# Kernel tuning notes

Hardware: AMD Instinct MI355X
Metric: run time of the kernel (lower is better)

## Reference

```python
import jax, jax.numpy as jnp
import numpy as np

N, M = 4096, 8192
IN_DIM, OUT_DIM = 4096, 1024
NUM_SAMPLE = 10


def setup_inputs() -> dict:
    key = jax.random.key(0)
    k1, k2, k3, k4, k5 = jax.random.split(key, 5)
    node_features = jax.random.normal(k1, (N, IN_DIM), dtype=jnp.float32)
    neighbor_features = jax.random.normal(k2, (M, IN_DIM), dtype=jnp.float32)
    # Xavier-ish scale for params
    weight = jax.random.normal(k3, (OUT_DIM, IN_DIM), dtype=jnp.float32) * (1.0 / np.sqrt(IN_DIM))
    attention_vector = jax.random.normal(k4, (2 * OUT_DIM, 1), dtype=jnp.float32) * 0.05
    neighbor_idx = jax.random.randint(k5, (N, NUM_SAMPLE), 0, M, dtype=jnp.int32)
    return {
        "node_features": node_features,
        "neighbor_features": neighbor_features,
        "weight": weight,
        "attention_vector": attention_vector,
        "neighbor_idx": neighbor_idx,
    }


def reference(node_features, neighbor_features, weight, attention_vector, neighbor_idx):
    # Linear transform: [N, out], [M, out]
    node_t = node_features @ weight.T
    neigh_t = neighbor_features @ weight.T

    # combined @ attention_vector decomposes:
    # cat([h_i, h_j]) @ a == h_i @ a1 + h_j @ a2  (same math, no [N,M,2*out] tensor)
    a1 = attention_vector[:OUT_DIM, 0]   # [out]
    a2 = attention_vector[OUT_DIM:, 0]   # [out]
    scores = jax.nn.leaky_relu((node_t @ a1)[:, None] + (neigh_t @ a2)[None, :],
                               negative_slope=0.2)  # [N, M]

    # Build dense 0/1 mask from sampled neighbor indices (ragged -> dense)
    rows = jnp.arange(N, dtype=jnp.int32)[:, None]                  # [N,1]
    mask = jnp.zeros((N, M), dtype=jnp.float32).at[rows, neighbor_idx].set(1.0)

    scores = jnp.where(mask == 0, -jnp.inf, scores)
    attn = jax.nn.softmax(scores, axis=1)           # masked softmax over neighbor pool
    return attn @ neigh_t                           # [N, out]
```

## Files before the change

kernel.cpp:

```cpp
#include <hip/hip_runtime.h>

#define IN_DIM  4096
#define OUT_DIM 1024
#define NN      4096
#define MM      8192
#define NSAMP   10

typedef __bf16 bf16x8 __attribute__((ext_vector_type(8)));
typedef float  fx4    __attribute__((ext_vector_type(4)));

__device__ __forceinline__ ushort f2bf(float f) {
    union { float f; unsigned u; } v; v.f = f;
    unsigned u = v.u;
    return (ushort)((u + 0x7FFFu + ((u >> 16) & 1u)) >> 16);
}
__device__ __forceinline__ float bf2f(ushort u) {
    union { unsigned u; float f; } v; v.u = ((unsigned)u) << 16;
    return v.f;
}

#define GLDS(g, l) __builtin_amdgcn_global_load_lds(                           \
    (const __attribute__((address_space(1))) unsigned*)(g),                    \
    (__attribute__((address_space(3))) unsigned*)(l), 16, 0, 0)

__global__ __launch_bounds__(256) void k_attvec(const float* __restrict__ W,
                                                const float* __restrict__ att,
                                                float* __restrict__ v1,
                                                float* __restrict__ v2,
                                                ushort* __restrict__ Wbf) {
    int k  = blockIdx.x * 256 + threadIdx.x;
    int o0 = blockIdx.y * 64;
    float s1 = 0.f, s2 = 0.f;
    for (int o = o0; o < o0 + 64; ++o) {
        float w = W[(size_t)o * IN_DIM + k];
        Wbf[(size_t)o * IN_DIM + k] = f2bf(w);
        s1 += att[o] * w;
        s2 += att[OUT_DIM + o] * w;
    }
    atomicAdd(&v1[k], s1);
    atomicAdd(&v2[k], s2);
}

__global__ __launch_bounds__(256) void k_rows(const float* __restrict__ node_f,
                                              const float* __restrict__ neigh_f,
                                              const float* __restrict__ v1,
                                              const float* __restrict__ v2,
                                              float* __restrict__ nalpha,
                                              float* __restrict__ nbeta,
                                              ushort* __restrict__ Abf) {
    int row = blockIdx.x;
    float s = 0.f;
    if (row < NN) {
        const float4* xr = reinterpret_cast<const float4*>(node_f + (size_t)row * IN_DIM);
        const float4* vr = reinterpret_cast<const float4*>(v1);
        for (int i = threadIdx.x; i < IN_DIM / 4; i += 256) {
            float4 a = xr[i], b = vr[i];
            s += a.x * b.x + a.y * b.y + a.z * b.z + a.w * b.w;
        }
    } else {
        int j = row - NN;
        const float4* xr = reinterpret_cast<const float4*>(neigh_f + (size_t)j * IN_DIM);
        const float4* vr = reinterpret_cast<const float4*>(v2);
        ushort4* yr = reinterpret_cast<ushort4*>(Abf + (size_t)j * IN_DIM);
        for (int i = threadIdx.x; i < IN_DIM / 4; i += 256) {
            float4 a = xr[i], b = vr[i];
            s += a.x * b.x + a.y * b.y + a.z * b.z + a.w * b.w;
            ushort4 o;
            o.x = f2bf(a.x); o.y = f2bf(a.y); o.z = f2bf(a.z); o.w = f2bf(a.w);
            yr[i] = o;
        }
    }
    for (int off = 32; off > 0; off >>= 1) s += __shfl_down(s, off, 64);
    __shared__ float ws[4];
    if ((threadIdx.x & 63) == 0) ws[threadIdx.x >> 6] = s;
    __syncthreads();
    if (threadIdx.x == 0) {
        float t = ws[0] + ws[1] + ws[2] + ws[3];
        if (row < NN) nalpha[row] = t; else nbeta[row - NN] = t;
    }
}

#define TM 128
#define TN 128
#define BK 32
#define KSPLIT (IN_DIM / 2)

__global__ __launch_bounds__(256, 4) void k_gemm(const ushort* __restrict__ A,
                                                 const ushort* __restrict__ B,
                                                 ushort* __restrict__ P) {
    __shared__ __align__(16) ushort As[TM * BK];
    __shared__ __align__(16) ushort Bs[TN * BK];
    const int tid  = threadIdx.x;
    const int lane = tid & 63;
    const int wave = tid >> 6;
    const int wm   = (wave >> 1) * 64;
    const int wn   = (wave & 1) * 64;
    const int bm   = blockIdx.x * TM;
    const int bn   = blockIdx.y * TN;
    const int kb   = blockIdx.z * KSPLIT;
    const int quad = lane >> 4;
    const int lrow = lane & 15;

    const int srow  = wave * 32 + (lane >> 2);
    const int skoff = (lane & 3) * 8;
    const ushort* gA = A + (size_t)(bm + srow) * IN_DIM + kb + skoff;
    const ushort* gB = B + (size_t)(bn + srow) * IN_DIM + kb + skoff;
    ushort* lA = As + wave * 1024;
    ushort* lB = Bs + wave * 1024;

    fx4 acc[4][4] = {};

    for (int k0 = 0; k0 < KSPLIT; k0 += BK) {
        GLDS(gA + k0,                lA);
        GLDS(gA + k0 + 16 * IN_DIM,  lA + 512);
        GLDS(gB + k0,                lB);
        GLDS(gB + k0 + 16 * IN_DIM,  lB + 512);
        __syncthreads();

        bf16x8 af[4], bfr[4];
#pragma unroll
        for (int mi = 0; mi < 4; ++mi)
            af[mi] = *reinterpret_cast<const bf16x8*>(As + (wm + mi * 16 + lrow) * BK + quad * 8);
#pragma unroll
        for (int ni = 0; ni < 4; ++ni)
            bfr[ni] = *reinterpret_cast<const bf16x8*>(Bs + (wn + ni * 16 + lrow) * BK + quad * 8);
#pragma unroll
        for (int mi = 0; mi < 4; ++mi)
#pragma unroll
            for (int ni = 0; ni < 4; ++ni)
                acc[mi][ni] = __builtin_amdgcn_mfma_f32_16x16x32_bf16(af[mi], bfr[ni], acc[mi][ni], 0, 0, 0);
        __syncthreads();
    }

    ushort* Pz = P + (size_t)blockIdx.z * MM * OUT_DIM;
#pragma unroll
    for (int mi = 0; mi < 4; ++mi)
#pragma unroll
        for (int ni = 0; ni < 4; ++ni) {
            int r = bm + wm + mi * 16 + quad * 4;
            int c = bn + wn + ni * 16 + lrow;
#pragma unroll
            for (int v = 0; v < 4; ++v)
                Pz[(size_t)(r + v) * OUT_DIM + c] = f2bf(acc[mi][ni][v]);
        }
}

__global__ __launch_bounds__(256) void k_aggregate(const ushort* __restrict__ P,
                                                   const float* __restrict__ nalpha,
                                                   const float* __restrict__ nbeta,
                                                   const int* __restrict__ nidx,
                                                   float* __restrict__ outp) {
    int row = blockIdx.x;
    __shared__ int   s_idx[NSAMP];
    __shared__ float s_w[NSAMP];
    if (threadIdx.x < 16) {
        int t = threadIdx.x;
        int j = (t < NSAMP) ? nidx[row * NSAMP + t] : -1;
        float score = -INFINITY;
        if (t < NSAMP) {
            float x = nalpha[row] + nbeta[j];
            score = x > 0.f ? x : 0.2f * x;
        }
        bool dup = false;
#pragma unroll
        for (int sIdx = 0; sIdx < NSAMP; ++sIdx) {
            int js = __shfl(j, sIdx, 16);
            if (sIdx < t && js == j) dup = true;
        }
        float mx = score;
#pragma unroll
        for (int off = 8; off > 0; off >>= 1) {
            float o = __shfl_xor(mx, off, 16);
            mx = o > mx ? o : mx;
        }
        float e = (t < NSAMP && !dup) ? expf(score - mx) : 0.f;
        float sum = e;
#pragma unroll
        for (int off = 8; off > 0; off >>= 1) sum += __shfl_xor(sum, off, 16);
        if (t < NSAMP) {
            s_idx[t] = j;
            s_w[t]   = e / sum;
        }
    }
    __syncthreads();
    int col = threadIdx.x * 4;
    float ax = 0.f, ay = 0.f, az = 0.f, aw = 0.f;
#pragma unroll
    for (int t = 0; t < NSAMP; ++t) {
        float w = s_w[t];
        size_t off = (size_t)s_idx[t] * OUT_DIM + col;
        ushort4 u0 = *reinterpret_cast<const ushort4*>(P + off);
        ushort4 u1 = *reinterpret_cast<const ushort4*>(P + (size_t)MM * OUT_DIM + off);
        ax += w * (bf2f(u0.x) + bf2f(u1.x));
        ay += w * (bf2f(u0.y) + bf2f(u1.y));
        az += w * (bf2f(u0.z) + bf2f(u1.z));
        aw += w * (bf2f(u0.w) + bf2f(u1.w));
    }
    float4 o; o.x = ax; o.y = ay; o.z = az; o.w = aw;
    *reinterpret_cast<float4*>(outp + (size_t)row * OUT_DIM + col) = o;
}

extern "C" void kernel_launch(void* const* d_in, const int* in_sizes, int n_in,
                              void* d_out, int out_size, void* d_ws, size_t ws_size,
                              hipStream_t stream) {
    const float* node_f  = (const float*)d_in[0];
    const float* neigh_f = (const float*)d_in[1];
    const float* W       = (const float*)d_in[2];
    const float* att     = (const float*)d_in[3];
    const int*   nidx    = (const int*)d_in[4];
    float* outp = (float*)d_out;

    char* ws = (char*)d_ws;
    ushort* Abf = (ushort*)ws;
    ushort* Wbf = (ushort*)(ws + 67108864);
    ushort* P   = (ushort*)(ws + 75497472);
    float*  v1     = (float*)(ws + 109051904);
    float*  v2     = v1 + IN_DIM;
    float*  nalpha = v2 + IN_DIM;
    float*  nbeta  = nalpha + NN;

    hipMemsetAsync(v1, 0, 2 * IN_DIM * sizeof(float), stream);

    k_attvec   <<<dim3(16, 16), 256, 0, stream>>>(W, att, v1, v2, Wbf);
    k_rows     <<<NN + MM,      256, 0, stream>>>(node_f, neigh_f, v1, v2, nalpha, nbeta, Abf);
    k_gemm     <<<dim3(MM / TM, OUT_DIM / TN, 2), 256, 0, stream>>>(Abf, Wbf, P);
    k_aggregate<<<NN,           256, 0, stream>>>(P, nalpha, nbeta, nidx, outp);
}
```

Measured before the change: 379.9 us.

## Retune prep kernels and restructure GEMM with BK64, LDS swizzle and block remap

The GEMM k-tile grows from 32 to 64, and LDS columns are XOR-swizzled to avoid bank conflicts on fragment reads. The 3D grid becomes a 1D grid with a remapping that interleaves workgroups, likely to spread them across XCDs for L2 locality. The row-reduction kernel now processes one row per wave, which removes the shared-memory reduction and the block barrier. The attvec kernel uses more blocks with fewer rows each to raise parallelism, at the cost of more atomics. Larger LDS tiles may reduce occupancy.

```diff
diff --git a/kernel.cpp b/kernel.cpp
--- a/kernel.cpp
+++ b/kernel.cpp
@@ -29,9 +29,10 @@
                                                 float* __restrict__ v2,
                                                 ushort* __restrict__ Wbf) {
     int k  = blockIdx.x * 256 + threadIdx.x;
-    int o0 = blockIdx.y * 64;
+    int o0 = blockIdx.y * 16;
     float s1 = 0.f, s2 = 0.f;
-    for (int o = o0; o < o0 + 64; ++o) {
+#pragma unroll
+    for (int o = o0; o < o0 + 16; ++o) {
         float w = W[(size_t)o * IN_DIM + k];
         Wbf[(size_t)o * IN_DIM + k] = f2bf(w);
         s1 += att[o] * w;
@@ -48,12 +49,14 @@
                                               float* __restrict__ nalpha,
                                               float* __restrict__ nbeta,
                                               ushort* __restrict__ Abf) {
-    int row = blockIdx.x;
+    int row  = blockIdx.x * 4 + (threadIdx.x >> 6);
+    int lane = threadIdx.x & 63;
     float s = 0.f;
     if (row < NN) {
         const float4* xr = reinterpret_cast<const float4*>(node_f + (size_t)row * IN_DIM);
         const float4* vr = reinterpret_cast<const float4*>(v1);
-        for (int i = threadIdx.x; i < IN_DIM / 4; i += 256) {
+#pragma unroll
+        for (int i = lane; i < IN_DIM / 4; i += 64) {
             float4 a = xr[i], b = vr[i];
             s += a.x * b.x + a.y * b.y + a.z * b.z + a.w * b.w;
         }
@@ -62,7 +65,8 @@
         const float4* xr = reinterpret_cast<const float4*>(neigh_f + (size_t)j * IN_DIM);
         const float4* vr = reinterpret_cast<const float4*>(v2);
         ushort4* yr = reinterpret_cast<ushort4*>(Abf + (size_t)j * IN_DIM);
-        for (int i = threadIdx.x; i < IN_DIM / 4; i += 256) {
+#pragma unroll
+        for (int i = lane; i < IN_DIM / 4; i += 64) {
             float4 a = xr[i], b = vr[i];
             s += a.x * b.x + a.y * b.y + a.z * b.z + a.w * b.w;
             ushort4 o;
@@ -70,19 +74,16 @@
             yr[i] = o;
         }
     }
+#pragma unroll
     for (int off = 32; off > 0; off >>= 1) s += __shfl_down(s, off, 64);
-    __shared__ float ws[4];
-    if ((threadIdx.x & 63) == 0) ws[threadIdx.x >> 6] = s;
-    __syncthreads();
-    if (threadIdx.x == 0) {
-        float t = ws[0] + ws[1] + ws[2] + ws[3];
-        if (row < NN) nalpha[row] = t; else nbeta[row - NN] = t;
+    if (lane == 0) {
+        if (row < NN) nalpha[row] = s; else nbeta[row - NN] = s;
     }
 }
 
 #define TM 128
 #define TN 128
-#define BK 32
+#define BK 64
 #define KSPLIT (IN_DIM / 2)
 
 __global__ __launch_bounds__(256, 4) void k_gemm(const ushort* __restrict__ A,
@@ -95,49 +96,63 @@
     const int wave = tid >> 6;
     const int wm   = (wave >> 1) * 64;
     const int wn   = (wave & 1) * 64;
-    const int bm   = blockIdx.x * TM;
-    const int bn   = blockIdx.y * TN;
-    const int kb   = blockIdx.z * KSPLIT;
-    const int quad = lane >> 4;
     const int lrow = lane & 15;
-
-    const int srow  = wave * 32 + (lane >> 2);
-    const int skoff = (lane & 3) * 8;
-    const ushort* gA = A + (size_t)(bm + srow) * IN_DIM + kb + skoff;
-    const ushort* gB = B + (size_t)(bn + srow) * IN_DIM + kb + skoff;
-    ushort* lA = As + wave * 1024;
-    ushort* lB = Bs + wave * 1024;
+    const int q    = lane >> 4;
+
+    const int bid = blockIdx.x;
+    const int wg  = (bid & 7) * 128 + (bid >> 3);
+    const int bx  = wg & 63;
+    const int by  = (wg >> 6) & 7;
+    const int bz  = wg >> 9;
+    const int bm  = bx * TM;
+    const int bn  = by * TN;
+    const int kb  = bz * KSPLIT;
+
+    const int sr  = wave * 32 + (lane >> 3);
+    const int sco = (((lane & 7) ^ (lane >> 3)) << 3);
+    const ushort* gA = A + (size_t)(bm + sr) * IN_DIM + kb + sco;
+    const ushort* gB = B + (size_t)(bn + sr) * IN_DIM + kb + sco;
+    ushort* lA = As + wave * 2048;
+    ushort* lB = Bs + wave * 2048;
+
+    const int c0u = ((q ^ (lrow & 7)) << 3);
 
     fx4 acc[4][4] = {};
 
     for (int k0 = 0; k0 < KSPLIT; k0 += BK) {
-        GLDS(gA + k0,                lA);
-        GLDS(gA + k0 + 16 * IN_DIM,  lA + 512);
-        GLDS(gB + k0,                lB);
-        GLDS(gB + k0 + 16 * IN_DIM,  lB + 512);
+#pragma unroll
+        for (int i = 0; i < 4; ++i)
+            GLDS(gA + k0 + (size_t)i * 8 * IN_DIM, lA + i * 512);
+#pragma unroll
+        for (int i = 0; i < 4; ++i)
+            GLDS(gB + k0 + (size_t)i * 8 * IN_DIM, lB + i * 512);
         __syncthreads();
 
-        bf16x8 af[4], bfr[4];
-#pragma unroll
-        for (int mi = 0; mi < 4; ++mi)
-            af[mi] = *reinterpret_cast<const bf16x8*>(As + (wm + mi * 16 + lrow) * BK + quad * 8);
-#pragma unroll
-        for (int ni = 0; ni < 4; ++ni)
-            bfr[ni] = *reinterpret_cast<const bf16x8*>(Bs + (wn + ni * 16 + lrow) * BK + quad * 8);
-#pragma unroll
-        for (int mi = 0; mi < 4; ++mi)
+#pragma unroll
+        for (int s = 0; s < 2; ++s) {
+            const int co = c0u ^ (s << 5);
+            bf16x8 af[4], bfr[4];
+#pragma unroll
+            for (int mi = 0; mi < 4; ++mi)
+                af[mi] = *reinterpret_cast<const bf16x8*>(As + (wm + mi * 16 + lrow) * BK + co);
 #pragma unroll
             for (int ni = 0; ni < 4; ++ni)
-                acc[mi][ni] = __builtin_amdgcn_mfma_f32_16x16x32_bf16(af[mi], bfr[ni], acc[mi][ni], 0, 0, 0);
+                bfr[ni] = *reinterpret_cast<const bf16x8*>(Bs + (wn + ni * 16 + lrow) * BK + co);
+#pragma unroll
+            for (int mi = 0; mi < 4; ++mi)
+#pragma unroll
+                for (int ni = 0; ni < 4; ++ni)
+                    acc[mi][ni] = __builtin_amdgcn_mfma_f32_16x16x32_bf16(af[mi], bfr[ni], acc[mi][ni], 0, 0, 0);
+        }
         __syncthreads();
     }
 
-    ushort* Pz = P + (size_t)blockIdx.z * MM * OUT_DIM;
+    ushort* Pz = P + (size_t)bz * MM * OUT_DIM;
 #pragma unroll
     for (int mi = 0; mi < 4; ++mi)
 #pragma unroll
         for (int ni = 0; ni < 4; ++ni) {
-            int r = bm + wm + mi * 16 + quad * 4;
+            int r = bm + wm + mi * 16 + q * 4;
             int c = bn + wn + ni * 16 + lrow;
 #pragma unroll
             for (int v = 0; v < 4; ++v)
@@ -221,8 +236,8 @@
 
     hipMemsetAsync(v1, 0, 2 * IN_DIM * sizeof(float), stream);
 
-    k_attvec   <<<dim3(16, 16), 256, 0, stream>>>(W, att, v1, v2, Wbf);
-    k_rows     <<<NN + MM,      256, 0, stream>>>(node_f, neigh_f, v1, v2, nalpha, nbeta, Abf);
-    k_gemm     <<<dim3(MM / TM, OUT_DIM / TN, 2), 256, 0, stream>>>(Abf, Wbf, P);
-    k_aggregate<<<NN,           256, 0, stream>>>(P, nalpha, nbeta, nidx, outp);
-}
+    k_attvec   <<<dim3(16, 64),   256, 0, stream>>>(W, att, v1, v2, Wbf);
+    k_rows     <<<(NN + MM) / 4,  256, 0, stream>>>(node_f, neigh_f, v1, v2, nalpha, nbeta, Abf);
+    k_gemm     <<<1024,           256, 0, stream>>>(Abf, Wbf, P);
+    k_aggregate<<<NN,             256, 0, stream>>>(P, nalpha, nbeta, nidx, outp);
+}
```

After: 395.2 us. +4.0%, slower.
